# Kernel tuning notes

Measured on AMD Instinct MI355X. Metric: run time of the kernel, lower is better.

Reference implementation:

```python
import math
import jax, jax.numpy as jnp
import numpy as np

B, S, D, H = 4, 1024, 512, 8
DK = D // H


def lin(x, W, b):
    # torch nn.Linear: y = x @ W.T + b, W: [out, in]
    return jnp.einsum('...i,oi->...o', x, W) + b


def layer_norm(x, scale, bias, eps=1e-5):
    m = jnp.mean(x, axis=-1, keepdims=True)
    v = jnp.var(x, axis=-1, keepdims=True)
    return (x - m) / jnp.sqrt(v + eps) * scale + bias


def mha(q_in, k_in, v_in, Wq, bq, Wk, bk, Wv, bv, Wo, bo, gammas, mask, zero_pad):
    b, s, _ = q_in.shape
    q = lin(q_in, Wq, bq).reshape(b, s, H, DK).transpose(0, 2, 1, 3)  # bhsd
    k = lin(k_in, Wk, bk).reshape(b, s, H, DK).transpose(0, 2, 1, 3)
    v = lin(v_in, Wv, bv).reshape(b, s, H, DK).transpose(0, 2, 1, 3)
    scores = jnp.einsum('bhid,bhjd->bhij', q, k) / math.sqrt(DK)
    # no-grad distance-decay branch
    s_ = jnp.where(mask, scores, jnp.float32(-1e32))
    s_ = jax.nn.softmax(s_, axis=-1) * mask
    distcum = jnp.cumsum(s_, axis=-1)
    disttotal = jnp.sum(s_, axis=-1, keepdims=True)
    idx = jnp.arange(s)
    pos = jnp.abs(idx[None, :] - idx[:, None]).astype(jnp.float32)[None, None]  # |i-j|
    dist = jax.lax.stop_gradient(jnp.sqrt(jnp.clip((disttotal - distcum) * pos, 0.0, None)))
    gamma = -jax.nn.softplus(gammas)[None]  # [1,h,1,1]
    total_effect = jnp.clip(jnp.exp(dist * gamma), 1e-5, 1e5)
    scores = scores * total_effect
    # NOTE: original code calls scores.masked_fill(...) without assignment (no-op);
    # faithfully NOT re-masking before this softmax.
    att = jax.nn.softmax(scores, axis=-1)
    if zero_pad:
        att = att.at[:, :, 0, :].set(0.0)
    out = jnp.einsum('bhij,bhjd->bhid', att, v).transpose(0, 2, 1, 3).reshape(b, s, D)
    return lin(out, Wo, bo)


def setup_inputs() -> dict:
    key = jax.random.key(0)
    ks = jax.random.split(key, 32)
    ki = iter(range(32))

    def w(shape, scale=0.02):
        return jax.random.normal(ks[next(ki)], shape, jnp.float32) * scale

    inp = {
        'q_emb': jax.random.normal(ks[next(ki)], (B, S, D), jnp.float32),
        'qa_emb': jax.random.normal(ks[next(ki)], (B, S, D), jnp.float32),
    }
    for blk in (1, 2, 3):
        inp[f'Wq{blk}'] = w((D, D)); inp[f'bq{blk}'] = jnp.zeros((D,), jnp.float32)
        if blk == 3:
            inp['Wk3'] = w((D, D)); inp['bk3'] = jnp.zeros((D,), jnp.float32)
        inp[f'Wv{blk}'] = w((D, D)); inp[f'bv{blk}'] = jnp.zeros((D,), jnp.float32)
        inp[f'Wo{blk}'] = w((D, D)); inp[f'bo{blk}'] = jnp.zeros((D,), jnp.float32)
        inp[f'g{blk}'] = w((H, 1, 1), 0.5)
        inp[f'ls{blk}'] = jnp.ones((D,), jnp.float32)
        inp[f'lb{blk}'] = jnp.zeros((D,), jnp.float32)
    inp['know'] = jax.random.uniform(ks[next(ki)], (1, 1, D), jnp.float32, -1.0, 1.0)
    inp['Wlk'] = w((D, DK)); inp['b_lk'] = jnp.zeros((D,), jnp.float32)
    inp['Wlv'] = w((D, DK)); inp['b_lv'] = jnp.zeros((D,), jnp.float32)
    return inp


def reference(q_emb, qa_emb,
              Wq1, bq1, Wv1, bv1, Wo1, bo1, g1, ls1, lb1,
              Wq2, bq2, Wv2, bv2, Wo2, bo2, g2, ls2, lb2,
              Wq3, bq3, Wk3, bk3, Wv3, bv3, Wo3, bo3, g3, ls3, lb3,
              know, Wlk, b_lk, Wlv, b_lv):
    b, s, d = q_emb.shape
    ones = jnp.ones((s, s), dtype=bool)
    mask_peek = jnp.tril(ones, k=0)[None, None]   # peek_cur=True
    mask_nopeek = jnp.tril(ones, k=-1)[None, None]  # peek_cur=False

    # block1 / block2 share k and q projections (kq_same=True)
    hq = layer_norm(q_emb + mha(q_emb, q_emb, q_emb, Wq1, bq1, Wq1, bq1,
                                Wv1, bv1, Wo1, bo1, g1, mask_peek, False), ls1, lb1)
    ha = layer_norm(qa_emb + mha(qa_emb, qa_emb, qa_emb, Wq2, bq2, Wq2, bq2,
                                 Wv2, bv2, Wo2, bo2, g2, mask_peek, False), ls2, lb2)
    query = jnp.broadcast_to(know, (b, s, d))
    h = layer_norm(query + mha(query, hq, ha, Wq3, bq3, Wk3, bk3,
                               Wv3, bv3, Wo3, bo3, g3, mask_nopeek, True), ls3, lb3)

    # small multi-head combine
    key_t = jax.nn.sigmoid(lin(query.reshape(b, s, H, DK), Wlk, b_lk))  # [b,s,h,d]
    val_t = jax.nn.sigmoid(lin(h.reshape(b, s, H, DK), Wlv, b_lv))     # [b,s,h,d]
    beta = jnp.einsum('bshd,bsd->bsh', key_t, q_emb)
    alpha = jax.nn.softmax(beta, axis=-1)
    out = jnp.einsum('bsh,bshd->bsd', alpha, val_t)
    return out
```

## Files before the change

### kernel.cpp

```cpp
#include <hip/hip_runtime.h>
#include <math.h>

#define BB 4
#define S 1024
#define D 512
#define H 8
#define DKH 64

#define ATT_LD 1032
#define LOG2E 1.4426950408889634f

typedef __attribute__((ext_vector_type(8))) short bf16x8;
typedef __attribute__((ext_vector_type(4))) float f32x4;

#if __has_builtin(__builtin_amdgcn_exp2f)
#define EXP2(x) __builtin_amdgcn_exp2f(x)
#else
#define EXP2(x) exp2f(x)
#endif
#if __has_builtin(__builtin_amdgcn_sqrtf)
#define SQRTF(x) __builtin_amdgcn_sqrtf(x)
#else
#define SQRTF(x) sqrtf(x)
#endif
#if __has_builtin(__builtin_amdgcn_rcpf)
#define RCPF(x) __builtin_amdgcn_rcpf(x)
#else
#define RCPF(x) (1.0f / (x))
#endif

__device__ __forceinline__ unsigned short f2bf(float f){
  unsigned int u = __float_as_uint(f);
  u += 0x7FFFu + ((u >> 16) & 1u);
  return (unsigned short)(u >> 16);
}
__device__ __forceinline__ unsigned short f2bf_rhu(float f){
  return (unsigned short)((__float_as_uint(f) + 0x8000u) >> 16);
}
__device__ __forceinline__ unsigned int pk_rhu(float lo, float hi){
  unsigned int a = __float_as_uint(lo) + 0x8000u;
  unsigned int b = __float_as_uint(hi) + 0x8000u;
#if __has_builtin(__builtin_amdgcn_perm)
  return __builtin_amdgcn_perm(b, a, 0x07060302u);
#else
  return (a >> 16) | (b & 0xffff0000u);
#endif
}
__device__ __forceinline__ float bf2f(unsigned int v){
  return __uint_as_float(v << 16);
}
__device__ __forceinline__ f32x4 MFMA(bf16x8 a, bf16x8 b, f32x4 c){
  return __builtin_amdgcn_mfma_f32_16x16x32_bf16(a, b, c, 0, 0, 0);
}
__device__ __forceinline__ void gl_lds16(const void* g, void* l){
  __builtin_amdgcn_global_load_lds(
      (const __attribute__((address_space(1))) void*)g,
      (__attribute__((address_space(3))) void*)l, 16, 0, 0);
}

__device__ __forceinline__ float blk_sum(float* r, int t, float v){
  r[t] = v; __syncthreads();
  for (int s = 128; s > 0; s >>= 1){
    if (t < s) r[t] += r[t + s];
    __syncthreads();
  }
  float res = r[0]; __syncthreads();
  return res;
}

struct GemmJobs {
  const unsigned short* A[4];
  const unsigned short* W[4];
  const float* bias[4];
  void* C[4];
};
template<int OUTBF>
__global__ __launch_bounds__(256) void mfma_gemm_b(GemmJobs jb)
{
  __shared__ __align__(16) short As[128][32];
  __shared__ __align__(16) short Ws[128][32];
  const int t = threadIdx.x;
  const int z = blockIdx.z;
  const int n0 = blockIdx.x * 128, m0 = blockIdx.y * 128;
  const unsigned short* A = jb.A[z];
  const unsigned short* W = jb.W[z];
  const float* bias = jb.bias[z];
  const int w = t >> 6, lane = t & 63;
  const int wm = (w >> 1) << 6, wn = (w & 1) << 6;
  const int lm = lane & 15, q = lane >> 4;
  const int r = t >> 2, cc = (t & 3) << 3;
  char* ldsA = ((char*)&As[0][0]) + w * 1024;
  char* ldsW = ((char*)&Ws[0][0]) + w * 1024;
  f32x4 acc[4][4];
  #pragma unroll
  for (int a_ = 0; a_ < 4; a_++)
    #pragma unroll
    for (int b_ = 0; b_ < 4; b_++)
      acc[a_][b_] = (f32x4){0.f, 0.f, 0.f, 0.f};
  for (int k0 = 0; k0 < D; k0 += 32){
    gl_lds16(&A[(size_t)(m0 + r)      * D + k0 + cc], ldsA);
    gl_lds16(&A[(size_t)(m0 + r + 64) * D + k0 + cc], ldsA + 4096);
    gl_lds16(&W[(size_t)(n0 + r)      * D + k0 + cc], ldsW);
    gl_lds16(&W[(size_t)(n0 + r + 64) * D + k0 + cc], ldsW + 4096);
    __syncthreads();
    bf16x8 af[4], bf[4];
    #pragma unroll
    for (int mt = 0; mt < 4; mt++) af[mt] = *(const bf16x8*)&As[wm + mt*16 + lm][q*8];
    #pragma unroll
    for (int nt = 0; nt < 4; nt++) bf[nt] = *(const bf16x8*)&Ws[wn + nt*16 + lm][q*8];
    #pragma unroll
    for (int mt = 0; mt < 4; mt++)
      #pragma unroll
      for (int nt = 0; nt < 4; nt++)
        acc[mt][nt] = MFMA(af[mt], bf[nt], acc[mt][nt]);
    __syncthreads();
  }
  #pragma unroll
  for (int nt = 0; nt < 4; nt++){
    const int n = n0 + wn + nt*16 + lm;
    const float bs = bias[n];
    #pragma unroll
    for (int mt = 0; mt < 4; mt++){
      const int mb = m0 + wm + mt*16 + (q << 2);
      f32x4 c = acc[mt][nt];
      #pragma unroll
      for (int rr = 0; rr < 4; rr++){
        float vv = c[rr] + bs;
        if (OUTBF)
          ((unsigned short*)jb.C[z])[(size_t)(mb + rr) * D + n] = f2bf(vv);
        else
          ((float*)jb.C[z])[(size_t)(mb + rr) * D + n] = vv;
      }
    }
  }
}

#define KS_LD 66
struct VTArgs { const unsigned short* v[2]; unsigned short* vt[2]; };
__global__ __launch_bounds__(256) void vt_kernel(VTArgs a)
{
  __shared__ unsigned short tile[64 * KS_LD];
  const int z = blockIdx.z, bh = blockIdx.y, b = bh >> 3, h = bh & 7;
  const int j0 = blockIdx.x * 64;
  const int t = threadIdx.x;
  const unsigned short* vp = a.v[z];
  unsigned short* vtp = a.vt[z] + (size_t)bh * 64 * S;
  #pragma unroll
  for (int p = 0; p < 2; p++){
    int lin = t + p * 256, row = lin >> 3, c8 = (lin & 7) << 3;
    *(uint4*)&tile[row * KS_LD + c8] =
      *(const uint4*)&vp[((size_t)b * S + j0 + row) * D + h * DKH + c8];
  }
  __syncthreads();
  #pragma unroll
  for (int p = 0; p < 2; p++){
    int lin = t + p * 256, d = lin >> 3, c8 = (lin & 7) << 3;
    unsigned short tmp[8];
    #pragma unroll
    for (int jx = 0; jx < 8; jx++) tmp[jx] = tile[(c8 + jx) * KS_LD + d];
    *(uint4*)&vtp[(size_t)d * S + j0 + c8] = *(const uint4*)tmp;
  }
}

struct FAArgs {
  const unsigned short* qk[2];
  const unsigned short* vt[2];
  unsigned short* ctx[2];
  const float* g[2];
  const float* c3;
  int diag, zero_pad;
};
template<int C3>
__global__ __launch_bounds__(256) void fused_attn(FAArgs a)
{
  __shared__ __align__(16) unsigned short att[16 * ATT_LD];
  __shared__ float ls2s[16];
  const int t = threadIdx.x;
  const int z = blockIdx.z;
  const int bh = blockIdx.y, b = bh >> 3, h = bh & 7;
  const int i0 = blockIdx.x * 16;
  const int w = t >> 6, lane = t & 63, lm = lane & 15, q = lane >> 4;
  const unsigned short* qkp = a.qk[z];
  const unsigned short* vtp = a.vt[z] + (size_t)bh * 64 * S;
  unsigned short* ctxp = a.ctx[z];
  float gm2;
  { float gv = a.g[z][h];
    gm2 = -((gv > 20.f) ? gv : log1pf(expf(gv))) * LOG2E; }

  if (!C3){
    bf16x8 af0 = *(const bf16x8*)&qkp[((size_t)b * S + i0 + lm) * D + h * DKH + q*8];
    bf16x8 af1 = *(const bf16x8*)&qkp[((size_t)b * S + i0 + lm) * D + h * DKH + 32 + q*8];
    for (int jc = 0; jc < S; jc += 64){
      const int jrow = jc + w*16 + lm;
      const size_t kb = ((size_t)b * S + jrow) * D + h * DKH;
      bf16x8 bv0 = *(const bf16x8*)&qkp[kb + q*8];
      bf16x8 bv1 = *(const bf16x8*)&qkp[kb + 32 + q*8];
      f32x4 acc = (f32x4){0.f, 0.f, 0.f, 0.f};
      acc = MFMA(af0, bv0, acc);
      acc = MFMA(af1, bv1, acc);
      #pragma unroll
      for (int rr = 0; rr < 4; rr++)
        att[(q*4 + rr) * ATT_LD + jc + w*16 + lm] = f2bf_rhu(acc[rr] * 0.125f);
    }
  }
  __syncthreads();

  const int jA0 = lane * 8, jB0 = 512 + lane * 8;

  float cH[16], erH[16];
  if (C3){
    const float* c3p = a.c3 + ((size_t)b * H + h) * S;
    #pragma unroll
    for (int sg = 0; sg < 2; sg++)
      #pragma unroll
      for (int p4 = 0; p4 < 2; p4++){
        float4 x = *(const float4*)&c3p[sg*512 + lane*8 + p4*4];
        cH[sg*8+p4*4+0] = x.x * LOG2E; cH[sg*8+p4*4+1] = x.y * LOG2E;
        cH[sg*8+p4*4+2] = x.z * LOG2E; cH[sg*8+p4*4+3] = x.w * LOG2E;
      }
    #pragma unroll
    for (int k = 0; k < 16; k++) erH[k] = EXP2(cH[k]);
  }

  auto decay_row = [&](const float (&c)[16], const float (&er)[16],
                       const int i, unsigned short* rowp, const int rl){
    const int jmax = i + a.diag;
    const bool skipB = (jmax < 512);
    float pl[16];
    float runA = 0.f;
    #pragma unroll
    for (int k = 0; k < 8; k++){
      float e = (jA0 + k <= jmax) ? er[k] : 0.f;
      runA += e; pl[k] = runA;
    }
    float sA = runA;
    #pragma unroll
    for (int off = 1; off < 64; off <<= 1){
      float u = __shfl_up(sA, off, 64);
      if (lane >= off) sA += u;
    }
    const float TA = __shfl(sA, 63, 64);
    float T = TA, sB = 0.f, runB = 0.f;
    if (!skipB){
      #pragma unroll
      for (int k = 0; k < 8; k++){
        float e = (jB0 + k <= jmax) ? er[8+k] : 0.f;
        runB += e; pl[8+k] = runB;
      }
      sB = runB;
      #pragma unroll
      for (int off = 1; off < 64; off <<= 1){
        float u = __shfl_up(sB, off, 64);
        if (lane >= off) sB += u;
      }
      T = TA + __shfl(sB, 63, 64);
    }
    const float inv1 = RCPF(T);
    const float cbaseA = (T - (sA - runA)) * inv1;
    const float fiA = (float)(i - jA0);
    float ls2 = 0.f;
    #pragma unroll
    for (int k = 0; k < 8; k++){
      float remn = fmaf(-pl[k], inv1, cbaseA);
      float pos  = fabsf(fiA - (float)k);
      float dist = SQRTF(fmaxf(remn * pos, 0.f));
      float eff  = fmaxf(EXP2(gm2 * dist), 1e-5f);
      float pp   = EXP2(c[k] * eff);
      ls2 += pp; pl[k] = pp;
    }
    if (!skipB){
      const float cbaseB = (T - (TA + sB - runB)) * inv1;
      const float fiB = (float)(i - jB0);
      #pragma unroll
      for (int k = 0; k < 8; k++){
        float remn = fmaf(-pl[8+k], inv1, cbaseB);
        float pos  = fabsf(fiB - (float)k);
        float dist = SQRTF(fmaxf(remn * pos, 0.f));
        float eff  = fmaxf(EXP2(gm2 * dist), 1e-5f);
        float pp   = EXP2(c[8+k] * eff);
        ls2 += pp; pl[8+k] = pp;
      }
    } else {
      #pragma unroll
      for (int k = 0; k < 8; k++){ pl[8+k] = er[8+k]; ls2 += er[8+k]; }
    }
    #pragma unroll
    for (int off = 1; off < 64; off <<= 1) ls2 += __shfl_xor(ls2, off, 64);
    if (lane == 0) ls2s[rl] = RCPF(ls2);
    #pragma unroll
    for (int sg = 0; sg < 2; sg++){
      uint4 o;
      o.x = pk_rhu(pl[sg*8+0], pl[sg*8+1]);
      o.y = pk_rhu(pl[sg*8+2], pl[sg*8+3]);
      o.z = pk_rhu(pl[sg*8+4], pl[sg*8+5]);
      o.w = pk_rhu(pl[sg*8+6], pl[sg*8+7]);
      *(uint4*)&rowp[sg*512 + lane*8] = o;
    }
  };

  for (int rloc = 0; rloc < 4; rloc++){
    const int rl = w*4 + rloc;
    const int i = i0 + rl;
    unsigned short* rowp = &att[rl * ATT_LD];
    if (C3 && a.zero_pad && i == 0){
      uint4 zz = make_uint4(0u,0u,0u,0u);
      *(uint4*)&rowp[jA0] = zz;
      *(uint4*)&rowp[jB0] = zz;
      if (lane == 0) ls2s[0] = 1.f;
      continue;
    }
    if (C3){
      decay_row(cH, erH, i, rowp, rl);
    } else {
      float c[16], er[16];
      #pragma unroll
      for (int sg = 0; sg < 2; sg++){
        uint4 u = *(const uint4*)&rowp[sg*512 + lane*8];
        unsigned int uu[4] = {u.x, u.y, u.z, u.w};
        #pragma unroll
        for (int mel = 0; mel < 4; mel++){
          c[sg*8 + mel*2]     = bf2f(uu[mel] & 0xffffu) * LOG2E;
          c[sg*8 + mel*2 + 1] = bf2f(uu[mel] >> 16) * LOG2E;
        }
      }
      #pragma unroll
      for (int k = 0; k < 16; k++) er[k] = EXP2(c[k]);
      decay_row(c, er, i, rowp, rl);
    }
  }
  __syncthreads();

  f32x4 acc = (f32x4){0.f,0.f,0.f,0.f};
  for (int kc = 0; kc < S; kc += 64){
    #pragma unroll
    for (int kft = 0; kft < 2; kft++){
      bf16x8 afv = *(const bf16x8*)&att[lm * ATT_LD + kc + kft*32 + q*8];
      bf16x8 bv  = *(const bf16x8*)&vtp[(size_t)(w*16 + lm) * S + kc + kft*32 + q*8];
      acc = MFMA(afv, bv, acc);
    }
  }
  #pragma unroll
  for (int rr = 0; rr < 4; rr++){
    const int rl = q*4 + rr;
    const float sc = ls2s[rl];
    const int row = i0 + rl;
    ctxp[((size_t)b * S + row) * D + h * DKH + w*16 + lm] = f2bf(acc[rr] * sc);
  }
}

struct LNJobs {
  const float* resid[2];
  const float* y[2];
  const float* ls[2];
  const float* lb[2];
  unsigned short* out[2];
  int bcast[2];
};
__global__ __launch_bounds__(256) void ln_residual_b(LNJobs j)
{
  const int z = blockIdx.y;
  const int r = blockIdx.x, t = threadIdx.x;
  __shared__ float red[256];
  const size_t base = (size_t)r * D;
  const float* resid = j.resid[z];
  const float* y = j.y[z];
  const int bcast = j.bcast[z];
  float r0 = bcast ? resid[t]       : resid[base + t];
  float r1 = bcast ? resid[t + 256] : resid[base + t + 256];
  float x0 = r0 + y[base + t];
  float x1 = r1 + y[base + t + 256];
  float mean = blk_sum(red, t, x0 + x1) * (1.0f / 512.0f);
  float d0 = x0 - mean, d1 = x1 - mean;
  float var = blk_sum(red, t, d0*d0 + d1*d1) * (1.0f / 512.0f);
  float inv = rsqrtf(var + 1e-5f);
  j.out[z][base + t]       = f2bf(d0 * inv * j.ls[z][t]       + j.lb[z][t]);
  j.out[z][base + t + 256] = f2bf(d1 * inv * j.ls[z][t + 256] + j.lb[z][t + 256]);
}

struct CvtJobs {
  const float* s[12];
  unsigned short* d[12];
  int n[12];
};
__global__ __launch_bounds__(256) void cvt_all(CvtJobs jb){
  const int z = blockIdx.y;
  const int n = jb.n[z];
  const float* s = jb.s[z];
  unsigned short* d = jb.d[z];
  for (int idx = blockIdx.x * 256 + threadIdx.x; idx < n; idx += gridDim.x * 256)
    d[idx] = f2bf(s[idx]);
}

__global__ __launch_bounds__(256) void know_kernel(
    const float* __restrict__ know, const float* __restrict__ Wq3,
    const float* __restrict__ bq3, float* __restrict__ q3,
    const float* __restrict__ Wlk, const float* __restrict__ blk_,
    float* __restrict__ keyt)
{
  if (blockIdx.x < 128){
    const int wv = (blockIdx.x * 256 + threadIdx.x) >> 6;
    const int lane = threadIdx.x & 63;
    const float* wr = Wq3 + (size_t)wv * 512 + lane * 8;
    const float* kr = know + lane * 8;
    float4 w0 = *(const float4*)&wr[0], w1 = *(const float4*)&wr[4];
    float4 k0 = *(const float4*)&kr[0], k1 = *(const float4*)&kr[4];
    float p = w0.x*k0.x + w0.y*k0.y + w0.z*k0.z + w0.w*k0.w
            + w1.x*k1.x + w1.y*k1.y + w1.z*k1.z + w1.w*k1.w;
    #pragma unroll
    for (int off = 1; off < 64; off <<= 1) p += __shfl_xor(p, off, 64);
    if (lane == 0) q3[wv] = p + bq3[wv];
  } else {
    int idx = (blockIdx.x - 128) * 256 + threadIdx.x;
    int h = idx >> 9, n = idx & 511;
    float acc = 0.f;
    for (int i = 0; i < 64; i++) acc += know[h * 64 + i] * Wlk[(size_t)n * 64 + i];
    keyt[idx] = 1.f / (1.f + __expf(-(acc + blk_[n])));
  }
}

__global__ __launch_bounds__(256) void scores3_kernel(
    const float* __restrict__ q3, const unsigned short* __restrict__ k3,
    float* __restrict__ c3)
{
  int idx = blockIdx.x * 256 + threadIdx.x;
  int j  = idx & (S - 1);
  int bh = idx >> 10;
  int h  = bh & 7, b = bh >> 3;
  const unsigned short* kp = k3 + ((size_t)b * S + j) * D + h * DKH;
  const float* qp = q3 + h * DKH;
  float acc = 0.f;
  #pragma unroll
  for (int d8 = 0; d8 < 64; d8 += 8){
    uint4 u = *(const uint4*)&kp[d8];
    unsigned int uu[4] = {u.x, u.y, u.z, u.w};
    #pragma unroll
    for (int mel = 0; mel < 4; mel++){
      acc += qp[d8 + 2*mel]     * bf2f(uu[mel] & 0xffffu);
      acc += qp[d8 + 2*mel + 1] * bf2f(uu[mel] >> 16);
    }
  }
  c3[idx] = acc * 0.125f;
}

__global__ __launch_bounds__(256) void alphas_kernel(
    const float* __restrict__ keyt, const float* __restrict__ q_emb,
    float* __restrict__ alpha)
{
  const int row = blockIdx.x * 4 + (threadIdx.x >> 6);
  const int l = threadIdx.x & 63;
  const int h = l >> 3, sub = l & 7;
  const float* qr = q_emb + (size_t)row * D;
  const float* kt = keyt + h * D;
  float p = 0.f;
  for (int d = sub; d < D; d += 8) p += kt[d] * qr[d];
  p += __shfl_xor(p, 1, 64);
  p += __shfl_xor(p, 2, 64);
  p += __shfl_xor(p, 4, 64);
  float m = p;
  m = fmaxf(m, __shfl_xor(m, 8, 64));
  m = fmaxf(m, __shfl_xor(m, 16, 64));
  m = fmaxf(m, __shfl_xor(m, 32, 64));
  float e = __expf(p - m);
  float ssum = e;
  ssum += __shfl_xor(ssum, 8, 64);
  ssum += __shfl_xor(ssum, 16, 64);
  ssum += __shfl_xor(ssum, 32, 64);
  if (sub == 0) alpha[(size_t)row * H + h] = e / ssum;
}

__global__ __launch_bounds__(256) void val_fused(
    const unsigned short* __restrict__ Ah,
    const unsigned short* __restrict__ Wv,
    const float* __restrict__ blv,
    const float* __restrict__ alpha,
    float* __restrict__ out)
{
  __shared__ __align__(16) short As[128][32];
  __shared__ __align__(16) short Ws[128][32];
  __shared__ float als[128];
  const int t = threadIdx.x;
  const int n0 = blockIdx.x * 128, m0 = blockIdx.y * 128;
  if (t < 128) als[t] = alpha[m0 + t];
  const int w = t >> 6, lane = t & 63;
  const int wm = (w >> 1) << 6, wn = (w & 1) << 6;
  const int lm = lane & 15, q = lane >> 4;
  const int r = t >> 2, cc = (t & 3) << 3;
  f32x4 acc[4][4];
  #pragma unroll
  for (int a_ = 0; a_ < 4; a_++)
    #pragma unroll
    for (int b_ = 0; b_ < 4; b_++)
      acc[a_][b_] = (f32x4){0.f, 0.f, 0.f, 0.f};
  for (int k0 = 0; k0 < 64; k0 += 32){
    *(uint4*)&As[r][cc]      = *(const uint4*)&Ah[(size_t)(m0 + r) * 64 + k0 + cc];
    *(uint4*)&As[r + 64][cc] = *(const uint4*)&Ah[(size_t)(m0 + r + 64) * 64 + k0 + cc];
    *(uint4*)&Ws[r][cc]      = *(const uint4*)&Wv[(size_t)(n0 + r) * 64 + k0 + cc];
    *(uint4*)&Ws[r + 64][cc] = *(const uint4*)&Wv[(size_t)(n0 + r + 64) * 64 + k0 + cc];
    __syncthreads();
    bf16x8 af[4], bf[4];
    #pragma unroll
    for (int mt = 0; mt < 4; mt++) af[mt] = *(const bf16x8*)&As[wm + mt*16 + lm][q*8];
    #pragma unroll
    for (int nt = 0; nt < 4; nt++) bf[nt] = *(const bf16x8*)&Ws[wn + nt*16 + lm][q*8];
    #pragma unroll
    for (int mt = 0; mt < 4; mt++)
      #pragma unroll
      for (int nt = 0; nt < 4; nt++)
        acc[mt][nt] = MFMA(af[mt], bf[nt], acc[mt][nt]);
    __syncthreads();
  }
  #pragma unroll
  for (int nt = 0; nt < 4; nt++){
    const int n = n0 + wn + nt*16 + lm;
    const float bs = blv[n];
    #pragma unroll
    for (int mt = 0; mt < 4; mt++){
      const int mb = m0 + wm + mt*16;
      f32x4 c = acc[mt][nt];
      float part = 0.f;
      #pragma unroll
      for (int rr = 0; rr < 4; rr++){
        const int ml = (mb - m0) + (q << 2) + rr;
        float sg = 1.f / (1.f + __expf(-(c[rr] + bs)));
        part += als[ml] * sg;
      }
      part += __shfl_xor(part, 16, 64);
      if ((q & 1) == 0){
        const int srow = (mb >> 3) + (q >> 1);
        out[(size_t)srow * D + n] = part;
      }
    }
  }
}

extern "C" void kernel_launch(void* const* d_in, const int* in_sizes, int n_in,
                              void* d_out, int out_size, void* d_ws, size_t ws_size,
                              hipStream_t stream) {
  const float* q_emb  = (const float*)d_in[0];
  const float* qa_emb = (const float*)d_in[1];
  const float* Wq1 = (const float*)d_in[2],  *bq1 = (const float*)d_in[3];
  const float* Wv1 = (const float*)d_in[4],  *bv1 = (const float*)d_in[5];
  const float* Wo1 = (const float*)d_in[6],  *bo1 = (const float*)d_in[7];
  const float* g1  = (const float*)d_in[8],  *ls1 = (const float*)d_in[9],  *lb1 = (const float*)d_in[10];
  const float* Wq2 = (const float*)d_in[11], *bq2 = (const float*)d_in[12];
  const float* Wv2 = (const float*)d_in[13], *bv2 = (const float*)d_in[14];
  const float* Wo2 = (const float*)d_in[15], *bo2 = (const float*)d_in[16];
  const float* g2  = (const float*)d_in[17], *ls2 = (const float*)d_in[18], *lb2 = (const float*)d_in[19];
  const float* Wq3 = (const float*)d_in[20], *bq3 = (const float*)d_in[21];
  const float* Wk3 = (const float*)d_in[22], *bk3 = (const float*)d_in[23];
  const float* Wv3 = (const float*)d_in[24], *bv3 = (const float*)d_in[25];
  const float* Wo3 = (const float*)d_in[26], *bo3 = (const float*)d_in[27];
  const float* g3  = (const float*)d_in[28], *ls3 = (const float*)d_in[29], *lb3 = (const float*)d_in[30];
  const float* know = (const float*)d_in[31];
  const float* Wlk  = (const float*)d_in[32], *b_lk = (const float*)d_in[33];
  const float* Wlv  = (const float*)d_in[34], *b_lv = (const float*)d_in[35];
  float* outp = (float*)d_out;

  const size_t NSD = (size_t)BB * S * D;
  unsigned short* p = (unsigned short*)d_ws;
  unsigned short* qk1b = p; p += NSD;
  unsigned short* v1b  = p; p += NSD;
  unsigned short* qk2b = p; p += NSD;
  unsigned short* v2b  = p; p += NSD;
  unsigned short* k3b  = p; p += NSD;
  unsigned short* v3b  = p; p += NSD;
  unsigned short* ctx1b= p; p += NSD;
  unsigned short* ctx2b= p; p += NSD;
  unsigned short* ctx3b= p; p += NSD;
  unsigned short* xqb  = p; p += NSD;
  unsigned short* xab  = p; p += NSD;
  unsigned short* hqb  = p; p += NSD;
  unsigned short* hab  = p; p += NSD;
  unsigned short* hfb  = p; p += NSD;
  unsigned short* vt1  = p; p += NSD;
  unsigned short* vt2  = p; p += NSD;
  unsigned short* vt3  = p; p += NSD;
  unsigned short* wb   = p; p += (size_t)9 * D * D;
  unsigned short* wlvb = p; p += (size_t)D * DKH;
  float* yv0   = (float*)p;
  float* yv1   = yv0 + NSD;
  float* q3    = yv1 + NSD;
  float* keyt  = q3 + 512;
  float* c3    = keyt + 4096;
  float* alpha = c3 + (size_t)BB * H * S;

  unsigned short* Wq1b = wb + 0*(size_t)D*D;
  unsigned short* Wv1b = wb + 1*(size_t)D*D;
  unsigned short* Wo1b = wb + 2*(size_t)D*D;
  unsigned short* Wq2b = wb + 3*(size_t)D*D;
  unsigned short* Wv2b = wb + 4*(size_t)D*D;
  unsigned short* Wo2b = wb + 5*(size_t)D*D;
  unsigned short* Wk3b = wb + 6*(size_t)D*D;
  unsigned short* Wv3b = wb + 7*(size_t)D*D;
  unsigned short* Wo3b = wb + 8*(size_t)D*D;

  CvtJobs jb;
  jb.s[0] = q_emb;  jb.d[0] = xqb;  jb.n[0] = (int)NSD;
  jb.s[1] = qa_emb; jb.d[1] = xab;  jb.n[1] = (int)NSD;
  jb.s[2] = Wq1; jb.d[2] = Wq1b; jb.n[2] = D*D;
  jb.s[3] = Wv1; jb.d[3] = Wv1b; jb.n[3] = D*D;
  jb.s[4] = Wo1; jb.d[4] = Wo1b; jb.n[4] = D*D;
  jb.s[5] = Wq2; jb.d[5] = Wq2b; jb.n[5] = D*D;
  jb.s[6] = Wv2; jb.d[6] = Wv2b; jb.n[6] = D*D;
  jb.s[7] = Wo2; jb.d[7] = Wo2b; jb.n[7] = D*D;
  jb.s[8] = Wk3; jb.d[8] = Wk3b; jb.n[8] = D*D;
  jb.s[9] = Wv3; jb.d[9] = Wv3b; jb.n[9] = D*D;
  jb.s[10] = Wo3; jb.d[10] = Wo3b; jb.n[10] = D*D;
  jb.s[11] = Wlv; jb.d[11] = wlvb; jb.n[11] = D*DKH;
  cvt_all<<<dim3(256, 12), 256, 0, stream>>>(jb);

  {
    GemmJobs g;
    g.A[0]=xqb; g.W[0]=Wq1b; g.bias[0]=bq1; g.C[0]=qk1b;
    g.A[1]=xqb; g.W[1]=Wv1b; g.bias[1]=bv1; g.C[1]=v1b;
    g.A[2]=xab; g.W[2]=Wq2b; g.bias[2]=bq2; g.C[2]=qk2b;
    g.A[3]=xab; g.W[3]=Wv2b; g.bias[3]=bv2; g.C[3]=v2b;
    mfma_gemm_b<1><<<dim3(4, 32, 4), 256, 0, stream>>>(g);
  }
  { VTArgs a; a.v[0]=v1b; a.v[1]=v2b; a.vt[0]=vt1; a.vt[1]=vt2;
    vt_kernel<<<dim3(16, 32, 2), 256, 0, stream>>>(a); }
  { FAArgs a;
    a.qk[0]=qk1b; a.qk[1]=qk2b; a.vt[0]=vt1; a.vt[1]=vt2;
    a.ctx[0]=ctx1b; a.ctx[1]=ctx2b; a.g[0]=g1; a.g[1]=g2;
    a.c3=nullptr; a.diag=0; a.zero_pad=0;
    fused_attn<0><<<dim3(64, 32, 2), 256, 0, stream>>>(a); }
  {
    GemmJobs g;
    g.A[0]=ctx1b; g.W[0]=Wo1b; g.bias[0]=bo1; g.C[0]=yv0;
    g.A[1]=ctx2b; g.W[1]=Wo2b; g.bias[1]=bo2; g.C[1]=yv1;
    g.A[2]=ctx1b; g.W[2]=Wo1b; g.bias[2]=bo1; g.C[2]=yv0;
    g.A[3]=ctx1b; g.W[3]=Wo1b; g.bias[3]=bo1; g.C[3]=yv0;
    mfma_gemm_b<0><<<dim3(4, 32, 2), 256, 0, stream>>>(g);
  }
  {
    LNJobs lj;
    lj.resid[0]=q_emb;  lj.y[0]=yv0; lj.ls[0]=ls1; lj.lb[0]=lb1; lj.out[0]=hqb; lj.bcast[0]=0;
    lj.resid[1]=qa_emb; lj.y[1]=yv1; lj.ls[1]=ls2; lj.lb[1]=lb2; lj.out[1]=hab; lj.bcast[1]=0;
    ln_residual_b<<<dim3(BB*S, 2), 256, 0, stream>>>(lj);
  }

  know_kernel<<<144, 256, 0, stream>>>(know, Wq3, bq3, q3, Wlk, b_lk, keyt);
  {
    GemmJobs g;
    g.A[0]=hqb; g.W[0]=Wk3b; g.bias[0]=bk3; g.C[0]=k3b;
    g.A[1]=hab; g.W[1]=Wv3b; g.bias[1]=bv3; g.C[1]=v3b;
    g.A[2]=hqb; g.W[2]=Wk3b; g.bias[2]=bk3; g.C[2]=k3b;
    g.A[3]=hqb; g.W[3]=Wk3b; g.bias[3]=bk3; g.C[3]=k3b;
    mfma_gemm_b<1><<<dim3(4, 32, 2), 256, 0, stream>>>(g);
  }
  { VTArgs a; a.v[0]=v3b; a.v[1]=v3b; a.vt[0]=vt3; a.vt[1]=vt3;
    vt_kernel<<<dim3(16, 32, 1), 256, 0, stream>>>(a); }
  scores3_kernel<<<128, 256, 0, stream>>>(q3, k3b, c3);
  { FAArgs a;
    a.qk[0]=k3b; a.qk[1]=k3b; a.vt[0]=vt3; a.vt[1]=vt3;
    a.ctx[0]=ctx3b; a.ctx[1]=ctx3b; a.g[0]=g3; a.g[1]=g3;
    a.c3=c3; a.diag=-1; a.zero_pad=1;
    fused_attn<1><<<dim3(64, 32, 1), 256, 0, stream>>>(a); }
  {
    GemmJobs g;
    g.A[0]=ctx3b; g.W[0]=Wo3b; g.bias[0]=bo3; g.C[0]=yv0;
    g.A[1]=ctx3b; g.W[1]=Wo3b; g.bias[1]=bo3; g.C[1]=yv0;
    g.A[2]=ctx3b; g.W[2]=Wo3b; g.bias[2]=bo3; g.C[2]=yv0;
    g.A[3]=ctx3b; g.W[3]=Wo3b; g.bias[3]=bo3; g.C[3]=yv0;
    mfma_gemm_b<0><<<dim3(4, 32, 1), 256, 0, stream>>>(g);
  }
  {
    LNJobs lj;
    lj.resid[0]=know; lj.y[0]=yv0; lj.ls[0]=ls3; lj.lb[0]=lb3; lj.out[0]=hfb; lj.bcast[0]=1;
    lj.resid[1]=know; lj.y[1]=yv0; lj.ls[1]=ls3; lj.lb[1]=lb3; lj.out[1]=hfb; lj.bcast[1]=1;
    ln_residual_b<<<dim3(BB*S, 1), 256, 0, stream>>>(lj);
  }

  alphas_kernel<<<1024, 256, 0, stream>>>(keyt, q_emb, alpha);
  val_fused<<<dim3(4, 256), 256, 0, stream>>>(hfb, wlvb, b_lv, alpha, outp);
}
```

Measured before the change: 438.9 us.

## Use DPP wave scans/reductions and register-prefetch K/V tiles in fused attention

Replaces the shuffle-based 64-lane prefix scans and reductions in the decay row computation with DPP row_shr adds plus readlane combination. This is meant to cut the LDS-backed ds_bpermute traffic those shuffles generate. Software-prefetches the next K and V tiles into registers in both MFMA loops so global load latency overlaps compute. Adds a launch-bounds occupancy hint of 4 blocks per CU, which may raise register pressure and risk spills.

```diff
diff --git a/kernel.cpp b/kernel.cpp
--- a/kernel.cpp
+++ b/kernel.cpp
@@ -56,6 +56,33 @@
   __builtin_amdgcn_global_load_lds(
       (const __attribute__((address_space(1))) void*)g,
       (__attribute__((address_space(3))) void*)l, 16, 0, 0);
+}
+
+template<int CTRL>
+__device__ __forceinline__ float dppadd(float v){
+  int s = __builtin_amdgcn_update_dpp(0, __float_as_int(v), CTRL, 0xf, 0xf, true);
+  return v + __int_as_float(s);
+}
+__device__ __forceinline__ float rdl(float v, int l){
+  return __int_as_float(__builtin_amdgcn_readlane(__float_as_int(v), l));
+}
+__device__ __forceinline__ void wave_scan64(float v, int lane, float& incl, float& total){
+  float r = dppadd<0x111>(v);
+  r = dppadd<0x112>(r);
+  r = dppadd<0x114>(r);
+  r = dppadd<0x118>(r);
+  float t0 = rdl(r, 15), t1 = rdl(r, 31), t2 = rdl(r, 47), t3 = rdl(r, 63);
+  const int row = lane >> 4;
+  float off = (row > 0 ? t0 : 0.f) + (row > 1 ? t1 : 0.f) + (row > 2 ? t2 : 0.f);
+  incl = r + off;
+  total = (t0 + t1) + (t2 + t3);
+}
+__device__ __forceinline__ float wave_sum64(float v){
+  float r = dppadd<0x111>(v);
+  r = dppadd<0x112>(r);
+  r = dppadd<0x114>(r);
+  r = dppadd<0x118>(r);
+  return (rdl(r, 15) + rdl(r, 31)) + (rdl(r, 47) + rdl(r, 63));
 }
 
 __device__ __forceinline__ float blk_sum(float* r, int t, float v){
@@ -171,7 +198,7 @@
   int diag, zero_pad;
 };
 template<int C3>
-__global__ __launch_bounds__(256) void fused_attn(FAArgs a)
+__global__ __launch_bounds__(256, 4) void fused_attn(FAArgs a)
 {
   __shared__ __align__(16) unsigned short att[16 * ATT_LD];
   __shared__ float ls2s[16];
@@ -188,19 +215,26 @@
     gm2 = -((gv > 20.f) ? gv : log1pf(expf(gv))) * LOG2E; }
 
   if (!C3){
-    bf16x8 af0 = *(const bf16x8*)&qkp[((size_t)b * S + i0 + lm) * D + h * DKH + q*8];
-    bf16x8 af1 = *(const bf16x8*)&qkp[((size_t)b * S + i0 + lm) * D + h * DKH + 32 + q*8];
+    const size_t rowbase = (size_t)b * S;
+    bf16x8 af0 = *(const bf16x8*)&qkp[(rowbase + i0 + lm) * D + h * DKH + q*8];
+    bf16x8 af1 = *(const bf16x8*)&qkp[(rowbase + i0 + lm) * D + h * DKH + 32 + q*8];
+    size_t kb = (rowbase + w*16 + lm) * D + h * DKH;
+    bf16x8 bv0 = *(const bf16x8*)&qkp[kb + q*8];
+    bf16x8 bv1 = *(const bf16x8*)&qkp[kb + 32 + q*8];
     for (int jc = 0; jc < S; jc += 64){
-      const int jrow = jc + w*16 + lm;
-      const size_t kb = ((size_t)b * S + jrow) * D + h * DKH;
-      bf16x8 bv0 = *(const bf16x8*)&qkp[kb + q*8];
-      bf16x8 bv1 = *(const bf16x8*)&qkp[kb + 32 + q*8];
+      bf16x8 nb0, nb1;
+      if (jc + 64 < S){
+        size_t kb2 = (rowbase + jc + 64 + w*16 + lm) * D + h * DKH;
+        nb0 = *(const bf16x8*)&qkp[kb2 + q*8];
+        nb1 = *(const bf16x8*)&qkp[kb2 + 32 + q*8];
+      }
       f32x4 acc = (f32x4){0.f, 0.f, 0.f, 0.f};
       acc = MFMA(af0, bv0, acc);
       acc = MFMA(af1, bv1, acc);
       #pragma unroll
       for (int rr = 0; rr < 4; rr++)
         att[(q*4 + rr) * ATT_LD + jc + w*16 + lm] = f2bf_rhu(acc[rr] * 0.125f);
+      bv0 = nb0; bv1 = nb1;
     }
   }
   __syncthreads();
@@ -233,13 +267,8 @@
       float e = (jA0 + k <= jmax) ? er[k] : 0.f;
       runA += e; pl[k] = runA;
     }
-    float sA = runA;
-    #pragma unroll
-    for (int off = 1; off < 64; off <<= 1){
-      float u = __shfl_up(sA, off, 64);
-      if (lane >= off) sA += u;
-    }
-    const float TA = __shfl(sA, 63, 64);
+    float sA, TA;
+    wave_scan64(runA, lane, sA, TA);
     float T = TA, sB = 0.f, runB = 0.f;
     if (!skipB){
       #pragma unroll
@@ -247,13 +276,9 @@
         float e = (jB0 + k <= jmax) ? er[8+k] : 0.f;
         runB += e; pl[8+k] = runB;
       }
-      sB = runB;
-      #pragma unroll
-      for (int off = 1; off < 64; off <<= 1){
-        float u = __shfl_up(sB, off, 64);
-        if (lane >= off) sB += u;
-      }
-      T = TA + __shfl(sB, 63, 64);
+      float TB;
+      wave_scan64(runB, lane, sB, TB);
+      T = TA + TB;
     }
     const float inv1 = RCPF(T);
     const float cbaseA = (T - (sA - runA)) * inv1;
@@ -284,8 +309,7 @@
       #pragma unroll
       for (int k = 0; k < 8; k++){ pl[8+k] = er[8+k]; ls2 += er[8+k]; }
     }
-    #pragma unroll
-    for (int off = 1; off < 64; off <<= 1) ls2 += __shfl_xor(ls2, off, 64);
+    ls2 = wave_sum64(ls2);
     if (lane == 0) ls2s[rl] = RCPF(ls2);
     #pragma unroll
     for (int sg = 0; sg < 2; sg++){
@@ -331,13 +355,20 @@
   __syncthreads();
 
   f32x4 acc = (f32x4){0.f,0.f,0.f,0.f};
+  const unsigned short* vrow = &vtp[(size_t)(w*16 + lm) * S];
+  bf16x8 bv0 = *(const bf16x8*)&vrow[q*8];
+  bf16x8 bv1 = *(const bf16x8*)&vrow[32 + q*8];
   for (int kc = 0; kc < S; kc += 64){
-    #pragma unroll
-    for (int kft = 0; kft < 2; kft++){
-      bf16x8 afv = *(const bf16x8*)&att[lm * ATT_LD + kc + kft*32 + q*8];
-      bf16x8 bv  = *(const bf16x8*)&vtp[(size_t)(w*16 + lm) * S + kc + kft*32 + q*8];
-      acc = MFMA(afv, bv, acc);
-    }
+    bf16x8 nb0, nb1;
+    if (kc + 64 < S){
+      nb0 = *(const bf16x8*)&vrow[kc + 64 + q*8];
+      nb1 = *(const bf16x8*)&vrow[kc + 96 + q*8];
+    }
+    bf16x8 a0 = *(const bf16x8*)&att[lm * ATT_LD + kc + q*8];
+    bf16x8 a1 = *(const bf16x8*)&att[lm * ATT_LD + kc + 32 + q*8];
+    acc = MFMA(a0, bv0, acc);
+    acc = MFMA(a1, bv1, acc);
+    bv0 = nb0; bv1 = nb1;
   }
   #pragma unroll
   for (int rr = 0; rr < 4; rr++){
@@ -406,8 +437,7 @@
     float4 k0 = *(const float4*)&kr[0], k1 = *(const float4*)&kr[4];
     float p = w0.x*k0.x + w0.y*k0.y + w0.z*k0.z + w0.w*k0.w
             + w1.x*k1.x + w1.y*k1.y + w1.z*k1.z + w1.w*k1.w;
-    #pragma unroll
-    for (int off = 1; off < 64; off <<= 1) p += __shfl_xor(p, off, 64);
+    p = wave_sum64(p);
     if (lane == 0) q3[wv] = p + bq3[wv];
   } else {
     int idx = (blockIdx.x - 128) * 256 + threadIdx.x;
```

Result: no change. 432.5 us (-1.5%).
